# Performance work log

Hardware: AMD Instinct MI355X
Metric: run time of the kernel (lower is better)

Reference implementation:

```python
import jax, jax.numpy as jnp
import numpy as np

N_EMBD = 768
N_HEAD = 12
EPS = 1e-5


def _layernorm(x, g, b):
    mu = jnp.mean(x, axis=-1, keepdims=True)
    var = jnp.var(x, axis=-1, keepdims=True)
    return (x - mu) * jax.lax.rsqrt(var + EPS) * g + b


def setup_inputs() -> dict:
    key = jax.random.key(0)
    ks = jax.random.split(key, 12)
    C = N_EMBD
    s = 0.02
    return {
        "x": jax.random.normal(ks[0], (1, 4096, C), dtype=jnp.float32),
        "ln1_g": jnp.ones((C,), jnp.float32),
        "ln1_b": jnp.zeros((C,), jnp.float32),
        "w_attn": jax.random.normal(ks[1], (C, 3 * C), jnp.float32) * s,
        "b_attn": jnp.zeros((3 * C,), jnp.float32),
        "w_ao": jax.random.normal(ks[2], (C, C), jnp.float32) * s,
        "b_ao": jnp.zeros((C,), jnp.float32),
        "ln2_g": jnp.ones((C,), jnp.float32),
        "ln2_b": jnp.zeros((C,), jnp.float32),
        "w_fc": jax.random.normal(ks[3], (C, 4 * C), jnp.float32) * s,
        "b_fc": jnp.zeros((4 * C,), jnp.float32),
        "w_proj": jax.random.normal(ks[4], (4 * C, C), jnp.float32) * s,
        "b_proj": jnp.zeros((C,), jnp.float32),
    }


def reference(x, ln1_g, ln1_b, w_attn, b_attn, w_ao, b_ao,
              ln2_g, ln2_b, w_fc, b_fc, w_proj, b_proj):
    B, T, C = x.shape
    H = N_HEAD
    D = C // H

    # ---- attention sub-block ----
    h = _layernorm(x, ln1_g, ln1_b)
    qkv = h @ w_attn + b_attn                      # [B,T,3C]
    q, k, v = jnp.split(qkv, 3, axis=-1)
    q = q.reshape(B, T, H, D).transpose(0, 2, 1, 3)  # [B,H,T,D]
    k = k.reshape(B, T, H, D).transpose(0, 2, 1, 3)
    v = v.reshape(B, T, H, D).transpose(0, 2, 1, 3)
    att = jnp.einsum('bhqd,bhkd->bhqk', q, k) * (1.0 / jnp.sqrt(jnp.float32(D)))
    att = jax.nn.softmax(att, axis=-1)             # no causal mask in source
    y = jnp.einsum('bhqk,bhkd->bhqd', att, v)      # [B,H,T,D]
    y = y.transpose(0, 2, 1, 3).reshape(B, T, C)
    x = x + y @ w_ao + b_ao

    # ---- MLP sub-block ----
    h = _layernorm(x, ln2_g, ln2_b)
    h = jax.nn.gelu(h @ w_fc + b_fc, approximate=False)  # torch F.gelu = exact
    x = x + h @ w_proj + b_proj
    return x
```

## Files before the change

### kernel.cpp

```cpp
#include <hip/hip_runtime.h>
#include <hip/hip_bf16.h>
#include <cstdint>
#include <cstddef>

typedef __hip_bfloat16 bf16;
typedef __attribute__((ext_vector_type(8))) short short8;
typedef __attribute__((ext_vector_type(4))) float f32x4;
typedef __attribute__((ext_vector_type(16))) float f32x16;

#define C_EMBD 768
#define C3     2304
#define T_SEQ  4096
#define NHEAD  12
#define KVSPLIT 2

__device__ __forceinline__ void load16(const void* g, void* lds) {
  __builtin_amdgcn_global_load_lds(
      (const __attribute__((address_space(1))) uint32_t*)g,
      (__attribute__((address_space(3))) uint32_t*)lds, 16, 0, 0);
}

__device__ __forceinline__ short f2bf_bits(float x) {
  union { bf16 h; short s; } u; u.h = __float2bfloat16(x); return u.s;
}

__device__ __forceinline__ float bfbits2f(short s) {
  union { uint32_t u; float f; } u; u.u = ((uint32_t)(unsigned short)s) << 16; return u.f;
}

__device__ __forceinline__ float max3f(float a, float b, float c) {
  float d;
  asm("v_max3_f32 %0, %1, %2, %3" : "=v"(d) : "v"(a), "v"(b), "v"(c));
  return d;
}

#if __has_builtin(__builtin_amdgcn_exp2f)
#define QK_SCALE (0.125f * 1.44269504088896340736f)
__device__ __forceinline__ float expx(float x) { return __builtin_amdgcn_exp2f(x); }
#else
#define QK_SCALE 0.125f
__device__ __forceinline__ float expx(float x) { return __expf(x); }
#endif

__global__ __launch_bounds__(256) void ln_kernel(const float* __restrict__ x,
    const float* __restrict__ g, const float* __restrict__ b, bf16* __restrict__ out) {
  const int row = blockIdx.x;
  const int tid = threadIdx.x;
  const int lane = tid & 63, wave = tid >> 6;
  const float* xr = x + (size_t)row * C_EMBD;
  float v[3];
  #pragma unroll
  for (int i = 0; i < 3; ++i) v[i] = xr[tid + i * 256];
  float s = v[0] + v[1] + v[2];
  #pragma unroll
  for (int o = 1; o < 64; o <<= 1) s += __shfl_xor(s, o, 64);
  __shared__ float red[4];
  if (lane == 0) red[wave] = s;
  __syncthreads();
  const float mu = (red[0] + red[1] + red[2] + red[3]) * (1.0f / C_EMBD);
  float d0 = v[0] - mu, d1 = v[1] - mu, d2 = v[2] - mu;
  float q = d0 * d0 + d1 * d1 + d2 * d2;
  #pragma unroll
  for (int o = 1; o < 64; o <<= 1) q += __shfl_xor(q, o, 64);
  __syncthreads();
  if (lane == 0) red[wave] = q;
  __syncthreads();
  const float var = (red[0] + red[1] + red[2] + red[3]) * (1.0f / C_EMBD);
  const float rs = rsqrtf(var + 1e-5f);
  #pragma unroll
  for (int i = 0; i < 3; ++i) {
    int c = tid + i * 256;
    out[(size_t)row * C_EMBD + c] = __float2bfloat16((v[i] - mu) * rs * g[c] + b[c]);
  }
}

__global__ __launch_bounds__(256) void transpose_kernel(const float* __restrict__ in,
    bf16* __restrict__ out, int R, int C) {
  __shared__ float tile[32][33];
  const int bx = blockIdx.x * 32;
  const int by = blockIdx.y * 32;
  const int tx = threadIdx.x, ty = threadIdx.y;
  #pragma unroll
  for (int i = 0; i < 32; i += 8)
    tile[ty + i][tx] = in[(size_t)(by + ty + i) * C + bx + tx];
  __syncthreads();
  #pragma unroll
  for (int i = 0; i < 32; i += 8)
    out[(size_t)(bx + ty + i) * R + by + tx] = __float2bfloat16(tile[tx][ty + i]);
}

template <int EPI>
__global__ __launch_bounds__(256, 2) void gemm_bt(
    const bf16* __restrict__ A, const bf16* __restrict__ BT,
    const float* __restrict__ bias, const float* __restrict__ res,
    void* __restrict__ outp, int M, int N, int K) {
  __shared__ __align__(16) short sA[128 * 32];
  __shared__ __align__(16) short sB[128 * 32];
  const int tid = threadIdx.x;
  const int wave = tid >> 6, lane = tid & 63;
  const int qr = lane >> 4, qm = lane & 15;
  const int wr = wave >> 1, wc = wave & 1;
  const int tM = blockIdx.y * 128, tN = blockIdx.x * 128;

  f32x4 acc[4][4] = {};

  const int srow = tid >> 2;
  const int scol = (tid & 3) * 8;
  const bf16* gA = A + (size_t)(tM + srow) * K + scol;
  const bf16* gB = BT + (size_t)(tN + srow) * K + scol;
  char* ldsAw = (char*)sA + wave * 1024;
  char* ldsBw = (char*)sB + wave * 1024;
  const size_t rowskip = (size_t)64 * K;

  const int nk = K >> 5;
  for (int k0 = 0; k0 < nk; ++k0) {
    __syncthreads();
    load16(gA, ldsAw);
    load16(gA + rowskip, ldsAw + 4096);
    load16(gB, ldsBw);
    load16(gB + rowskip, ldsBw + 4096);
    gA += 32; gB += 32;
    __syncthreads();
    short8 a[4], bb[4];
    #pragma unroll
    for (int i = 0; i < 4; ++i) {
      a[i]  = *(const short8*)&sA[(wr * 64 + i * 16 + qm) * 32 + qr * 8];
      bb[i] = *(const short8*)&sB[(wc * 64 + i * 16 + qm) * 32 + qr * 8];
    }
    #pragma unroll
    for (int mi = 0; mi < 4; ++mi)
      #pragma unroll
      for (int ni = 0; ni < 4; ++ni)
        acc[mi][ni] = __builtin_amdgcn_mfma_f32_16x16x32_bf16(a[mi], bb[ni], acc[mi][ni], 0, 0, 0);
  }

  float* outf = (float*)outp;
  bf16* outh = (bf16*)outp;
  #pragma unroll
  for (int mi = 0; mi < 4; ++mi) {
    #pragma unroll
    for (int ni = 0; ni < 4; ++ni) {
      const int col = tN + wc * 64 + ni * 16 + qm;
      const float bv = bias[col];
      #pragma unroll
      for (int r = 0; r < 4; ++r) {
        const int row = tM + wr * 64 + mi * 16 + qr * 4 + r;
        const size_t idx = (size_t)row * N + col;
        float v = acc[mi][ni][r] + bv;
        if constexpr (EPI == 1) {
          outf[idx] = v + res[idx];
        } else if constexpr (EPI == 2) {
          v = 0.5f * v * (1.0f + erff(v * 0.70710678118654752f));
          outh[idx] = __float2bfloat16(v);
        } else {
          outh[idx] = __float2bfloat16(v);
        }
      }
    }
  }
}

__global__ __launch_bounds__(256, 2) void attn_kernel(const bf16* __restrict__ qkv,
                                                      float* __restrict__ pacc,
                                                      float* __restrict__ pml) {
  __shared__ __align__(16) char sKb[2 * 8192];
  __shared__ __align__(16) char sVb[2 * 8192];
  __shared__ float sRed[4 * 32];

  const int tid = threadIdx.x;
  const int wave = tid >> 6, lane = tid & 63;
  const int qi = lane & 31;
  const int hi = lane >> 5;
  const int hi16 = hi * 16;
  const int head = blockIdx.y;
  const int z = blockIdx.z;
  const int qw = blockIdx.x * 128 + wave * 32;

  short8 qf[4];
  {
    const bf16* qrow = qkv + (size_t)(qw + qi) * C3 + head * 64;
    #pragma unroll
    for (int kd = 0; kd < 4; ++kd) {
      short8 v = *(const short8*)(qrow + kd * 16 + hi * 8);
      #pragma unroll
      for (int i = 0; i < 8; ++i) v[i] = f2bf_bits(bfbits2f(v[i]) * QK_SCALE);
      qf[kd] = v;
    }
  }

  f32x16 acc0 = {}, acc1 = {};
  float m = -3.0e38f, l = 0.f;
  short8 pfrag[4];

  const int nt = (T_SEQ / 64) / KVSPLIT;
  const size_t tilestep = (size_t)64 * C3;
  const size_t zoff = (size_t)z * nt * tilestep;
  const int ksrow = tid >> 3;
  const int kswz = ((tid & 7) ^ (ksrow & 7)) * 8;
  const bf16* gk_base = qkv + zoff + (size_t)ksrow * C3 + C_EMBD + head * 64 + kswz;
  const int vp = tid & 31;
  const int vd0 = (tid >> 5) * 8;
  const bf16* gv_base = qkv + zoff + (size_t)(2 * vp) * C3 + 2 * C_EMBD + head * 64 + vd0;

  const int krow0 = qi * 128;
  const int krow_swz = (qi & 7) << 4;
  const int d1 = 32 + qi;
  const int vs0 = ((qi & 7) ^ ((qi >> 3) & 7)) << 4;
  const int vs1 = ((d1 & 7) ^ ((d1 >> 3) & 7)) << 4;

  short8 v0 = *(const short8*)gv_base;
  short8 v1 = *(const short8*)(gv_base + C3);
  load16(gk_base, sKb + wave * 1024);
  load16(gk_base + (size_t)32 * C3, sKb + wave * 1024 + 4096);

  for (int t = 0; t < nt; ++t) {
    const int cur = t & 1;
    char* bK = sKb + cur * 8192;
    char* bV = sVb + cur * 8192;

    __syncthreads();

    #pragma unroll
    for (int j = 0; j < 8; ++j) {
      const int d = vd0 + j;
      const int vs = ((d & 7) ^ ((d >> 3) & 7)) << 4;
      const uint32_t packed = (uint32_t)(unsigned short)v0[j] |
                              ((uint32_t)(unsigned short)v1[j] << 16);
      *(uint32_t*)(bV + d * 128 + ((vp * 4) ^ vs)) = packed;
    }

    if (t + 1 < nt) {
      const bf16* gv = gv_base + (size_t)(t + 1) * tilestep;
      v0 = *(const short8*)gv;
      v1 = *(const short8*)(gv + C3);
      const bf16* gk = gk_base + (size_t)(t + 1) * tilestep;
      char* bKn = sKb + (cur ^ 1) * 8192;
      load16(gk, bKn + wave * 1024);
      load16(gk + (size_t)32 * C3, bKn + wave * 1024 + 4096);
    }

    f32x16 s0 = {}, s1 = {};
    __builtin_amdgcn_s_setprio(1);
    #pragma unroll
    for (int kd = 0; kd < 4; ++kd) {
      const int off = (kd * 32 + hi16) ^ krow_swz;
      short8 ka0 = *(const short8*)(bK + krow0 + off);
      short8 ka1 = *(const short8*)(bK + 4096 + krow0 + off);
      s0 = __builtin_amdgcn_mfma_f32_32x32x16_bf16(ka0, qf[kd], s0, 0, 0, 0);
      s1 = __builtin_amdgcn_mfma_f32_32x32x16_bf16(ka1, qf[kd], s1, 0, 0, 0);
    }

    if (t > 0) {
      char* bVp = sVb + (cur ^ 1) * 8192;
      #pragma unroll
      for (int kk = 0; kk < 4; ++kk) {
        const int voff = (kk * 32 + hi16);
        short8 vb0 = *(const short8*)(bVp + qi * 128 + (voff ^ vs0));
        short8 vb1 = *(const short8*)(bVp + d1 * 128 + (voff ^ vs1));
        acc0 = __builtin_amdgcn_mfma_f32_32x32x16_bf16(pfrag[kk], vb0, acc0, 0, 0, 0);
        acc1 = __builtin_amdgcn_mfma_f32_32x32x16_bf16(pfrag[kk], vb1, acc1, 0, 0, 0);
      }
    }
    __builtin_amdgcn_s_setprio(0);

    float t8[8];
    #pragma unroll
    for (int i = 0; i < 8; ++i) t8[i] = max3f(s0[i], s0[i + 8], s1[i]);
    float t4[4];
    #pragma unroll
    for (int i = 0; i < 4; ++i) t4[i] = max3f(t8[2 * i], t8[2 * i + 1], s1[8 + i]);
    float t2[2];
    #pragma unroll
    for (int i = 0; i < 2; ++i) t2[i] = max3f(t4[2 * i], t4[2 * i + 1], s1[12 + i]);
    const float t1 = max3f(t2[0], t2[1], s1[14]);
    const float tmx = fmaxf(t1, s1[15]);
    float pmax;
    {
      float a0 = tmx, a1 = tmx;
      asm("v_permlane32_swap_b32 %0, %1" : "+v"(a0), "+v"(a1));
      pmax = fmaxf(a0, a1);
    }

    if (__any(pmax - m > 8.0f)) {
      const float mn = fmaxf(m, pmax);
      const float sc = expx(m - mn);
      l *= sc;
      if (lane < 32) sRed[wave * 32 + qi] = sc;
      #pragma unroll
      for (int r = 0; r < 16; ++r) {
        const float sv = sRed[wave * 32 + ((r & 3) + 8 * (r >> 2) + hi * 4)];
        acc0[r] *= sv; acc1[r] *= sv;
      }
      m = mn;
    }

    float red[16];
    #pragma unroll
    for (int r = 0; r < 16; ++r) { s0[r] = expx(s0[r] - m); s1[r] = expx(s1[r] - m); }
    #pragma unroll
    for (int r = 0; r < 16; ++r) red[r] = s0[r] + s1[r];
    #pragma unroll
    for (int w = 8; w >= 1; w >>= 1)
      #pragma unroll
      for (int r = 0; r < w; ++r) red[r] += red[r + w];
    {
      float a0 = red[0], a1 = red[0];
      asm("v_permlane32_swap_b32 %0, %1" : "+v"(a0), "+v"(a1));
      l += a0 + a1;
    }

    #pragma unroll
    for (int b = 0; b < 2; ++b) {
      const f32x16 sb = b ? s1 : s0;
      uint32_t pk[8];
      #pragma unroll
      for (int g = 0; g < 4; ++g) {
        asm("v_cvt_pk_bf16_f32 %0, %1, %2" : "=v"(pk[2 * g])     : "v"(sb[4 * g + 0]), "v"(sb[4 * g + 1]));
        asm("v_cvt_pk_bf16_f32 %0, %1, %2" : "=v"(pk[2 * g + 1]) : "v"(sb[4 * g + 2]), "v"(sb[4 * g + 3]));
      }
      #pragma unroll
      for (int kbl = 0; kbl < 2; ++kbl) {
        uint32_t w0 = pk[4 * kbl + 0], w2 = pk[4 * kbl + 2];
        asm("v_permlane32_swap_b32 %0, %1" : "+v"(w0), "+v"(w2));
        uint32_t w1 = pk[4 * kbl + 1], w3 = pk[4 * kbl + 3];
        asm("v_permlane32_swap_b32 %0, %1" : "+v"(w1), "+v"(w3));
        union { uint32_t u[4]; short8 v; } pu;
        pu.u[0] = w0; pu.u[1] = w1; pu.u[2] = w2; pu.u[3] = w3;
        pfrag[b * 2 + kbl] = pu.v;
      }
    }
  }

  __syncthreads();
  {
    char* bVl = sVb + ((nt - 1) & 1) * 8192;
    __builtin_amdgcn_s_setprio(1);
    #pragma unroll
    for (int kk = 0; kk < 4; ++kk) {
      const int voff = (kk * 32 + hi16);
      short8 vb0 = *(const short8*)(bVl + qi * 128 + (voff ^ vs0));
      short8 vb1 = *(const short8*)(bVl + d1 * 128 + (voff ^ vs1));
      acc0 = __builtin_amdgcn_mfma_f32_32x32x16_bf16(pfrag[kk], vb0, acc0, 0, 0, 0);
      acc1 = __builtin_amdgcn_mfma_f32_32x32x16_bf16(pfrag[kk], vb1, acc1, 0, 0, 0);
    }
    __builtin_amdgcn_s_setprio(0);
  }

  float* pa = pacc + ((size_t)z * T_SEQ + qw) * C_EMBD + head * 64;
  #pragma unroll
  for (int r = 0; r < 16; ++r) {
    const int q = (r & 3) + 8 * (r >> 2) + hi * 4;
    pa[(size_t)q * C_EMBD + qi]      = acc0[r];
    pa[(size_t)q * C_EMBD + 32 + qi] = acc1[r];
  }
  if (lane < 32) {
    float2* mlp = (float2*)pml;
    mlp[((size_t)z * NHEAD + head) * T_SEQ + qw + qi] = make_float2(m, l);
  }
}

__global__ __launch_bounds__(256) void attn_combine(const float* __restrict__ pacc,
    const float* __restrict__ pml, bf16* __restrict__ out) {
  const int q = blockIdx.x;
  const int tid = threadIdx.x;
  const float2* mlp = (const float2*)pml;
  #pragma unroll
  for (int i = 0; i < 3; ++i) {
    const int c = tid + i * 256;
    const int h = c >> 6;
    const float2 ml0 = mlp[(size_t)h * T_SEQ + q];
    const float2 ml1 = mlp[((size_t)NHEAD + h) * T_SEQ + q];
    const float M = fmaxf(ml0.x, ml1.x);
    const float w0 = expx(ml0.x - M), w1 = expx(ml1.x - M);
    const float inv = 1.0f / (ml0.y * w0 + ml1.y * w1);
    const float a0 = pacc[(size_t)q * C_EMBD + c];
    const float a1 = pacc[(size_t)T_SEQ * C_EMBD + (size_t)q * C_EMBD + c];
    out[(size_t)q * C_EMBD + c] = __float2bfloat16((a0 * w0 + a1 * w1) * inv);
  }
}

extern "C" void kernel_launch(void* const* d_in, const int* in_sizes, int n_in,
                              void* d_out, int out_size, void* d_ws, size_t ws_size,
                              hipStream_t stream) {
  const float* x      = (const float*)d_in[0];
  const float* ln1_g  = (const float*)d_in[1];
  const float* ln1_b  = (const float*)d_in[2];
  const float* w_attn = (const float*)d_in[3];
  const float* b_attn = (const float*)d_in[4];
  const float* w_ao   = (const float*)d_in[5];
  const float* b_ao   = (const float*)d_in[6];
  const float* ln2_g  = (const float*)d_in[7];
  const float* ln2_b  = (const float*)d_in[8];
  const float* w_fc   = (const float*)d_in[9];
  const float* b_fc   = (const float*)d_in[10];
  const float* w_proj = (const float*)d_in[11];
  const float* b_proj = (const float*)d_in[12];

  char* ws = (char*)d_ws;
  size_t off = 0;
  auto alloc = [&](size_t nbytes) {
    char* p = ws + off;
    off += (nbytes + 255) & ~(size_t)255;
    return p;
  };
  bf16* wT_attn = (bf16*)alloc((size_t)C3 * C_EMBD * 2);
  bf16* wT_ao   = (bf16*)alloc((size_t)C_EMBD * C_EMBD * 2);
  bf16* wT_fc   = (bf16*)alloc((size_t)4 * C_EMBD * C_EMBD * 2);
  bf16* wT_proj = (bf16*)alloc((size_t)C_EMBD * 4 * C_EMBD * 2);
  bf16* h       = (bf16*)alloc((size_t)T_SEQ * C_EMBD * 2);
  bf16* qkv     = (bf16*)alloc((size_t)T_SEQ * C3 * 2);
  bf16* y       = (bf16*)alloc((size_t)T_SEQ * C_EMBD * 2);
  float* x1     = (float*)alloc((size_t)T_SEQ * C_EMBD * 4);
  bf16* hf      = (bf16*)alloc((size_t)T_SEQ * 4 * C_EMBD * 2);
  float* pml    = (float*)alloc((size_t)KVSPLIT * NHEAD * T_SEQ * 2 * 4);
  float* pacc   = (float*)hf;
  (void)ws_size; (void)in_sizes; (void)n_in; (void)out_size;

  const dim3 tb(32, 8);
  transpose_kernel<<<dim3(C3 / 32, C_EMBD / 32), tb, 0, stream>>>(w_attn, wT_attn, C_EMBD, C3);
  transpose_kernel<<<dim3(C_EMBD / 32, C_EMBD / 32), tb, 0, stream>>>(w_ao, wT_ao, C_EMBD, C_EMBD);
  transpose_kernel<<<dim3(4 * C_EMBD / 32, C_EMBD / 32), tb, 0, stream>>>(w_fc, wT_fc, C_EMBD, 4 * C_EMBD);
  transpose_kernel<<<dim3(C_EMBD / 32, 4 * C_EMBD / 32), tb, 0, stream>>>(w_proj, wT_proj, 4 * C_EMBD, C_EMBD);

  ln_kernel<<<T_SEQ, 256, 0, stream>>>(x, ln1_g, ln1_b, h);
  gemm_bt<0><<<dim3(C3 / 128, T_SEQ / 128), 256, 0, stream>>>(h, wT_attn, b_attn, nullptr, qkv,
                                                              T_SEQ, C3, C_EMBD);
  attn_kernel<<<dim3(T_SEQ / 128, NHEAD, KVSPLIT), 256, 0, stream>>>(qkv, pacc, pml);
  attn_combine<<<T_SEQ, 256, 0, stream>>>(pacc, pml, y);
  gemm_bt<1><<<dim3(C_EMBD / 128, T_SEQ / 128), 256, 0, stream>>>(y, wT_ao, b_ao, x, x1,
                                                                  T_SEQ, C_EMBD, C_EMBD);
  ln_kernel<<<T_SEQ, 256, 0, stream>>>(x1, ln2_g, ln2_b, h);
  gemm_bt<2><<<dim3(4 * C_EMBD / 128, T_SEQ / 128), 256, 0, stream>>>(h, wT_fc, b_fc, nullptr, hf,
                                                                      T_SEQ, 4 * C_EMBD, C_EMBD);
  gemm_bt<1><<<dim3(C_EMBD / 128, T_SEQ / 128), 256, 0, stream>>>(hf, wT_proj, b_proj, x1,
                                                                  (float*)d_out, T_SEQ, C_EMBD,
                                                                  4 * C_EMBD);
}
```

Baseline: 261.3 us.

## Split-K the MLP projection GEMM and merge weight transposes into one launch

The final projection GEMM (K=3072, only 192 output tiles) is split into two K halves over a z grid dimension. Each half writes fp32 partials into reused buffers (d_out and the qkv workspace), and a new combine kernel adds the partials, residual and bias. This is meant to raise occupancy on the many-CU device for a GEMM that launches too few blocks, at the cost of extra partial-sum memory traffic and one more launch. Separately, the four weight-transpose launches are merged into one kernel that dispatches on the block index, to cut launch overhead.

```diff
diff --git a/kernel.cpp b/kernel.cpp
--- a/kernel.cpp
+++ b/kernel.cpp
@@ -74,11 +74,21 @@
   }
 }
 
-__global__ __launch_bounds__(256) void transpose_kernel(const float* __restrict__ in,
-    bf16* __restrict__ out, int R, int C) {
+__global__ __launch_bounds__(256) void transpose4_kernel(
+    const float* __restrict__ wA, bf16* __restrict__ oA,
+    const float* __restrict__ wB, bf16* __restrict__ oB,
+    const float* __restrict__ wC, bf16* __restrict__ oC,
+    const float* __restrict__ wD, bf16* __restrict__ oD) {
   __shared__ float tile[32][33];
-  const int bx = blockIdx.x * 32;
-  const int by = blockIdx.y * 32;
+  int b = blockIdx.x;
+  const float* in; bf16* out; int R, C;
+  if (b < 1728)      { in = wA; out = oA; R = 768;  C = 2304; }
+  else if (b < 2304) { b -= 1728; in = wB; out = oB; R = 768;  C = 768;  }
+  else if (b < 4608) { b -= 2304; in = wC; out = oC; R = 768;  C = 3072; }
+  else               { b -= 4608; in = wD; out = oD; R = 3072; C = 768;  }
+  const int ntx = C / 32;
+  const int bx = (b % ntx) * 32;
+  const int by = (b / ntx) * 32;
   const int tx = threadIdx.x, ty = threadIdx.y;
   #pragma unroll
   for (int i = 0; i < 32; i += 8)
@@ -93,7 +103,7 @@
 __global__ __launch_bounds__(256, 2) void gemm_bt(
     const bf16* __restrict__ A, const bf16* __restrict__ BT,
     const float* __restrict__ bias, const float* __restrict__ res,
-    void* __restrict__ outp, int M, int N, int K) {
+    void* __restrict__ outp, float* __restrict__ outp2, int M, int N, int Ks, int Kst) {
   __shared__ __align__(16) short sA[128 * 32];
   __shared__ __align__(16) short sB[128 * 32];
   const int tid = threadIdx.x;
@@ -101,18 +111,19 @@
   const int qr = lane >> 4, qm = lane & 15;
   const int wr = wave >> 1, wc = wave & 1;
   const int tM = blockIdx.y * 128, tN = blockIdx.x * 128;
+  const int z = (EPI == 4) ? blockIdx.z : 0;
 
   f32x4 acc[4][4] = {};
 
   const int srow = tid >> 2;
   const int scol = (tid & 3) * 8;
-  const bf16* gA = A + (size_t)(tM + srow) * K + scol;
-  const bf16* gB = BT + (size_t)(tN + srow) * K + scol;
+  const bf16* gA = A + (size_t)z * Ks + (size_t)(tM + srow) * Kst + scol;
+  const bf16* gB = BT + (size_t)z * Ks + (size_t)(tN + srow) * Kst + scol;
   char* ldsAw = (char*)sA + wave * 1024;
   char* ldsBw = (char*)sB + wave * 1024;
-  const size_t rowskip = (size_t)64 * K;
-
-  const int nk = K >> 5;
+  const size_t rowskip = (size_t)64 * Kst;
+
+  const int nk = Ks >> 5;
   for (int k0 = 0; k0 < nk; ++k0) {
     __syncthreads();
     load16(gA, ldsAw);
@@ -136,18 +147,21 @@
 
   float* outf = (float*)outp;
   bf16* outh = (bf16*)outp;
+  float* po = (EPI == 4) ? ((z == 0) ? (float*)outp : outp2) : nullptr;
   #pragma unroll
   for (int mi = 0; mi < 4; ++mi) {
     #pragma unroll
     for (int ni = 0; ni < 4; ++ni) {
       const int col = tN + wc * 64 + ni * 16 + qm;
-      const float bv = bias[col];
+      const float bv = (EPI == 4) ? 0.f : bias[col];
       #pragma unroll
       for (int r = 0; r < 4; ++r) {
         const int row = tM + wr * 64 + mi * 16 + qr * 4 + r;
         const size_t idx = (size_t)row * N + col;
         float v = acc[mi][ni][r] + bv;
-        if constexpr (EPI == 1) {
+        if constexpr (EPI == 4) {
+          po[idx] = v;
+        } else if constexpr (EPI == 1) {
           outf[idx] = v + res[idx];
         } else if constexpr (EPI == 2) {
           v = 0.5f * v * (1.0f + erff(v * 0.70710678118654752f));
@@ -157,6 +171,19 @@
         }
       }
     }
+  }
+}
+
+__global__ __launch_bounds__(256) void splitk_combine(const float* p0,
+    const float* __restrict__ p1, const float* __restrict__ res,
+    const float* __restrict__ bias, float* out) {
+  const int row = blockIdx.x;
+  const int tid = threadIdx.x;
+  #pragma unroll
+  for (int i = 0; i < 3; ++i) {
+    const int c = tid + i * 256;
+    const size_t idx = (size_t)row * C_EMBD + c;
+    out[idx] = p0[idx] + p1[idx] + res[idx] + bias[c];
   }
 }
 
@@ -414,25 +441,27 @@
   bf16* hf      = (bf16*)alloc((size_t)T_SEQ * 4 * C_EMBD * 2);
   float* pml    = (float*)alloc((size_t)KVSPLIT * NHEAD * T_SEQ * 2 * 4);
   float* pacc   = (float*)hf;
+  float* pp0    = (float*)d_out;
+  float* pp1    = (float*)qkv;
   (void)ws_size; (void)in_sizes; (void)n_in; (void)out_size;
 
-  const dim3 tb(32, 8);
-  transpose_kernel<<<dim3(C3 / 32, C_EMBD / 32), tb, 0, stream>>>(w_attn, wT_attn, C_EMBD, C3);
-  transpose_kernel<<<dim3(C_EMBD / 32, C_EMBD / 32), tb, 0, stream>>>(w_ao, wT_ao, C_EMBD, C_EMBD);
-  transpose_kernel<<<dim3(4 * C_EMBD / 32, C_EMBD / 32), tb, 0, stream>>>(w_fc, wT_fc, C_EMBD, 4 * C_EMBD);
-  transpose_kernel<<<dim3(C_EMBD / 32, 4 * C_EMBD / 32), tb, 0, stream>>>(w_proj, wT_proj, 4 * C_EMBD, C_EMBD);
+  transpose4_kernel<<<6912, dim3(32, 8), 0, stream>>>(w_attn, wT_attn, w_ao, wT_ao,
+                                                      w_fc, wT_fc, w_proj, wT_proj);
 
   ln_kernel<<<T_SEQ, 256, 0, stream>>>(x, ln1_g, ln1_b, h);
   gemm_bt<0><<<dim3(C3 / 128, T_SEQ / 128), 256, 0, stream>>>(h, wT_attn, b_attn, nullptr, qkv,
-                                                              T_SEQ, C3, C_EMBD);
+                                                              nullptr, T_SEQ, C3, C_EMBD, C_EMBD);
   attn_kernel<<<dim3(T_SEQ / 128, NHEAD, KVSPLIT), 256, 0, stream>>>(qkv, pacc, pml);
   attn_combine<<<T_SEQ, 256, 0, stream>>>(pacc, pml, y);
   gemm_bt<1><<<dim3(C_EMBD / 128, T_SEQ / 128), 256, 0, stream>>>(y, wT_ao, b_ao, x, x1,
-                                                                  T_SEQ, C_EMBD, C_EMBD);
+                                                                  nullptr, T_SEQ, C_EMBD,
+                                                                  C_EMBD, C_EMBD);
   ln_kernel<<<T_SEQ, 256, 0, stream>>>(x1, ln2_g, ln2_b, h);
   gemm_bt<2><<<dim3(4 * C_EMBD / 128, T_SEQ / 128), 256, 0, stream>>>(h, wT_fc, b_fc, nullptr, hf,
-                                                                      T_SEQ, 4 * C_EMBD, C_EMBD);
-  gemm_bt<1><<<dim3(C_EMBD / 128, T_SEQ / 128), 256, 0, stream>>>(hf, wT_proj, b_proj, x1,
-                                                                  (float*)d_out, T_SEQ, C_EMBD,
-                                                                  4 * C_EMBD);
-}
+                                                                      nullptr, T_SEQ, 4 * C_EMBD,
+                                                                      C_EMBD, C_EMBD);
+  gemm_bt<4><<<dim3(C_EMBD / 128, T_SEQ / 128, 2), 256, 0, stream>>>(hf, wT_proj, nullptr, nullptr,
+                                                                     pp0, pp1, T_SEQ, C_EMBD,
+                                                                     2 * C_EMBD, 4 * C_EMBD);
+  splitk_combine<<<T_SEQ, 256, 0, stream>>>(pp0, pp1, x1, b_proj, (float*)d_out);
+}
```

Result: faster. 235.9 us (-9.7%).
